# Optimization experiments

Measured on AMD Instinct MI355X. Metric: run time of the kernel, lower is better.

Reference implementation:

```python
import jax, jax.numpy as jnp
import numpy as np

# bitsandbytes NF4 codebook (16 quantile values in [-1, 1])
NF4 = jnp.array([
    -1.0, -0.6961928009986877, -0.5250730514526367, -0.39491748809814453,
    -0.28444138169288635, -0.18477343022823334, -0.09105003625154495, 0.0,
    0.07958029955625534, 0.16093020141124725, 0.24611230194568634,
    0.33791524171829224, 0.44070982933044434, 0.5626170039176941,
    0.7229568362236328, 1.0], dtype=jnp.float32)
BLOCK = 64  # bnb default quantization blocksize


def dequant_nf4(codes, absmax):
    """codes: int array of 4-bit indices, absmax: per-64-elem-block scale."""
    flat = NF4[codes.reshape(-1)]                      # codebook lookup
    flat = flat.reshape(-1, BLOCK) * absmax[:, None]   # per-block rescale
    return flat.reshape(codes.shape)


def setup_inputs() -> dict:
    key = jax.random.key(0)
    k1, k2, k3, k4, k5 = jax.random.split(key, 5)
    B, S, IN, OUT, R = 4, 2048, 4096, 4096, 8
    x = jax.random.normal(k1, (B, S, IN), dtype=jnp.float32)
    codes_A = jax.random.randint(k2, (R, IN), 0, 16, dtype=jnp.int32)
    absmax_A = jax.random.uniform(k3, (R * IN // BLOCK,), dtype=jnp.float32)
    codes_B = jax.random.randint(k4, (OUT, R), 0, 16, dtype=jnp.int32)
    absmax_B = jax.random.uniform(k5, (OUT * R // BLOCK,), dtype=jnp.float32)
    return {"x": x, "codes_A": codes_A, "absmax_A": absmax_A,
            "codes_B": codes_B, "absmax_B": absmax_B}


def reference(x, codes_A, absmax_A, codes_B, absmax_B):
    SCALING = 32.0 / 8.0  # alpha / rank
    W_A = dequant_nf4(codes_A, absmax_A)   # [rank, in]
    W_B = dequant_nf4(codes_B, absmax_B)   # [out, rank]
    interm = jnp.einsum('bsi,ri->bsr', x, W_A)          # lora_A: x @ W_A^T
    out = jnp.einsum('bsr,or->bso', interm, W_B)        # lora_B
    return out * SCALING
```

## Files before the change

kernel.cpp:

```cpp
#include <hip/hip_runtime.h>


static __device__ __constant__ float NF4_TBL[16] = {
    -1.0f, -0.6961928009986877f, -0.5250730514526367f, -0.39491748809814453f,
    -0.28444138169288635f, -0.18477343022823334f, -0.09105003625154495f, 0.0f,
    0.07958029955625534f, 0.16093020141124725f, 0.24611230194568634f,
    0.33791524171829224f, 0.44070982933044434f, 0.5626170039176941f,
    0.7229568362236328f, 1.0f};

__global__ void nf4_dequant_kernel(const int* __restrict__ codesA,
                                   const float* __restrict__ absA,
                                   const int* __restrict__ codesB,
                                   const float* __restrict__ absB,
                                   float* __restrict__ wA,
                                   float* __restrict__ wBt,
                                   int n) {
    int id = blockIdx.x * blockDim.x + threadIdx.x;
    if (id < n) {
        wA[id] = NF4_TBL[codesA[id] & 15] * absA[id >> 6];
        const int r = id >> 12;
        const int o = id & 4095;
        wBt[id] = NF4_TBL[codesB[o * 8 + r] & 15] * absB[o >> 3];
    }
}

__global__ __launch_bounds__(256) void lora_fused_kernel(
    const float* __restrict__ x,
    const float* __restrict__ wA,
    const float* __restrict__ wBt,
    float* __restrict__ out) {
    __shared__ float interm_s[8][8];

    const int t    = threadIdx.x;
    const int wave = t >> 6;
    const int lane = t & 63;
    const int row0 = blockIdx.x * 8;
    const int r0   = row0 + 2 * wave;

    const float4* __restrict__ x0  = (const float4*)(x + (size_t)r0 * 4096);
    const float4* __restrict__ x1  = x0 + 1024;
    const float4* __restrict__ wA4 = (const float4*)wA;

    float acc0[8], acc1[8];
    #pragma unroll
    for (int r = 0; r < 8; ++r) { acc0[r] = 0.f; acc1[r] = 0.f; }

    #pragma unroll 2
    for (int c = 0; c < 16; ++c) {
        const int idx = lane + 64 * c;
        const float4 xa = x0[idx];
        const float4 xb = x1[idx];
        #pragma unroll
        for (int r = 0; r < 8; ++r) {
            const float4 w = wA4[r * 1024 + idx];
            acc0[r] += xa.x * w.x + xa.y * w.y + xa.z * w.z + xa.w * w.w;
            acc1[r] += xb.x * w.x + xb.y * w.y + xb.z * w.z + xb.w * w.w;
        }
    }

    #pragma unroll
    for (int r = 0; r < 8; ++r) {
        float v0 = acc0[r], v1 = acc1[r];
        #pragma unroll
        for (int off = 32; off > 0; off >>= 1) {
            v0 += __shfl_down(v0, off, 64);
            v1 += __shfl_down(v1, off, 64);
        }
        if (lane == 0) {
            interm_s[2 * wave][r]     = v0;
            interm_s[2 * wave + 1][r] = v1;
        }
    }
    __syncthreads();

    float ims[8][8];
    #pragma unroll
    for (int m = 0; m < 8; ++m)
        #pragma unroll
        for (int r = 0; r < 8; ++r) {
            const float v = interm_s[m][r] * 4.0f;
            ims[m][r] = __int_as_float(
                __builtin_amdgcn_readfirstlane(__float_as_int(v)));
        }

    const float4* __restrict__ wt = (const float4*)wBt;

    #pragma unroll 1
    for (int k = 0; k < 4; ++k) {
        const int og = t + 256 * k;
        float4 w[8];
        #pragma unroll
        for (int r = 0; r < 8; ++r) w[r] = wt[r * 1024 + og];

        #pragma unroll
        for (int m = 0; m < 8; ++m) {
            float4 s;
            s.x = ims[m][0] * w[0].x + ims[m][1] * w[1].x + ims[m][2] * w[2].x
                + ims[m][3] * w[3].x + ims[m][4] * w[4].x + ims[m][5] * w[5].x
                + ims[m][6] * w[6].x + ims[m][7] * w[7].x;
            s.y = ims[m][0] * w[0].y + ims[m][1] * w[1].y + ims[m][2] * w[2].y
                + ims[m][3] * w[3].y + ims[m][4] * w[4].y + ims[m][5] * w[5].y
                + ims[m][6] * w[6].y + ims[m][7] * w[7].y;
            s.z = ims[m][0] * w[0].z + ims[m][1] * w[1].z + ims[m][2] * w[2].z
                + ims[m][3] * w[3].z + ims[m][4] * w[4].z + ims[m][5] * w[5].z
                + ims[m][6] * w[6].z + ims[m][7] * w[7].z;
            s.w = ims[m][0] * w[0].w + ims[m][1] * w[1].w + ims[m][2] * w[2].w
                + ims[m][3] * w[3].w + ims[m][4] * w[4].w + ims[m][5] * w[5].w
                + ims[m][6] * w[6].w + ims[m][7] * w[7].w;
            ((float4*)(out + (size_t)(row0 + m) * 4096))[og] = s;
        }
    }
}

extern "C" void kernel_launch(void* const* d_in, const int* in_sizes, int n_in,
                              void* d_out, int out_size, void* d_ws, size_t ws_size,
                              hipStream_t stream) {
    const float* x        = (const float*)d_in[0];
    const int*   codes_A  = (const int*)d_in[1];
    const float* absmax_A = (const float*)d_in[2];
    const int*   codes_B  = (const int*)d_in[3];
    const float* absmax_B = (const float*)d_in[4];
    float* out = (float*)d_out;

    constexpr int NW = 8 * 4096;
    float* wA  = (float*)d_ws;
    float* wBt = (float*)d_ws + NW;

    nf4_dequant_kernel<<<(NW + 255) / 256, 256, 0, stream>>>(
        codes_A, absmax_A, codes_B, absmax_B, wA, wBt, NW);

    lora_fused_kernel<<<8192 / 8, 256, 0, stream>>>(x, wA, wBt, out);
}
```

Baseline: 259.3 us.

## Split K dimension across waves with 16-lane row groups for lora_A stage

```diff
diff --git a/kernel.cpp b/kernel.cpp
--- a/kernel.cpp
+++ b/kernel.cpp
@@ -29,30 +29,33 @@
     const float* __restrict__ wA,
     const float* __restrict__ wBt,
     float* __restrict__ out) {
-    __shared__ float interm_s[8][8];
+    __shared__ float p_s[4][8][8];
+    __shared__ float im_s[8][8];
 
     const int t    = threadIdx.x;
     const int wave = t >> 6;
     const int lane = t & 63;
+    const int g    = lane >> 4;
+    const int l16  = lane & 15;
     const int row0 = blockIdx.x * 8;
-    const int r0   = row0 + 2 * wave;
 
-    const float4* __restrict__ x0  = (const float4*)(x + (size_t)r0 * 4096);
-    const float4* __restrict__ x1  = x0 + 1024;
-    const float4* __restrict__ wA4 = (const float4*)wA;
+    const float4* __restrict__ x0 =
+        (const float4*)(x + (size_t)(row0 + 2 * g) * 4096) + wave * 256;
+    const float4* __restrict__ x1 = x0 + 1024;
+    const float4* __restrict__ wq = (const float4*)wA + wave * 256;
 
     float acc0[8], acc1[8];
     #pragma unroll
     for (int r = 0; r < 8; ++r) { acc0[r] = 0.f; acc1[r] = 0.f; }
 
     #pragma unroll 2
-    for (int c = 0; c < 16; ++c) {
-        const int idx = lane + 64 * c;
+    for (int s = 0; s < 16; ++s) {
+        const int idx = s * 16 + l16;
         const float4 xa = x0[idx];
         const float4 xb = x1[idx];
         #pragma unroll
         for (int r = 0; r < 8; ++r) {
-            const float4 w = wA4[r * 1024 + idx];
+            const float4 w = wq[r * 1024 + idx];
             acc0[r] += xa.x * w.x + xa.y * w.y + xa.z * w.z + xa.w * w.w;
             acc1[r] += xb.x * w.x + xb.y * w.y + xb.z * w.z + xb.w * w.w;
         }
@@ -62,14 +65,21 @@
     for (int r = 0; r < 8; ++r) {
         float v0 = acc0[r], v1 = acc1[r];
         #pragma unroll
-        for (int off = 32; off > 0; off >>= 1) {
-            v0 += __shfl_down(v0, off, 64);
-            v1 += __shfl_down(v1, off, 64);
+        for (int off = 8; off > 0; off >>= 1) {
+            v0 += __shfl_down(v0, off, 16);
+            v1 += __shfl_down(v1, off, 16);
         }
-        if (lane == 0) {
-            interm_s[2 * wave][r]     = v0;
-            interm_s[2 * wave + 1][r] = v1;
+        if (l16 == 0) {
+            p_s[wave][2 * g][r]     = v0;
+            p_s[wave][2 * g + 1][r] = v1;
         }
+    }
+    __syncthreads();
+
+    if (t < 64) {
+        const int m = t >> 3, r = t & 7;
+        im_s[m][r] = (p_s[0][m][r] + p_s[1][m][r] +
+                      p_s[2][m][r] + p_s[3][m][r]) * 4.0f;
     }
     __syncthreads();
 
@@ -77,11 +87,9 @@
     #pragma unroll
     for (int m = 0; m < 8; ++m)
         #pragma unroll
-        for (int r = 0; r < 8; ++r) {
-            const float v = interm_s[m][r] * 4.0f;
+        for (int r = 0; r < 8; ++r)
             ims[m][r] = __int_as_float(
-                __builtin_amdgcn_readfirstlane(__float_as_int(v)));
-        }
+                __builtin_amdgcn_readfirstlane(__float_as_int(im_s[m][r])));
 
     const float4* __restrict__ wt = (const float4*)wBt;
 
```

Measured after the change: 257.1 us. No clear change (-0.9%).

## Split fused LoRA kernel into separate A-projection and B-projection kernels

Applied to the files above, without the earlier changes.

```diff
diff --git a/kernel.cpp b/kernel.cpp
--- a/kernel.cpp
+++ b/kernel.cpp
@@ -24,20 +24,15 @@
     }
 }
 
-__global__ __launch_bounds__(256) void lora_fused_kernel(
+__global__ __launch_bounds__(256) void lora_a_kernel(
     const float* __restrict__ x,
     const float* __restrict__ wA,
-    const float* __restrict__ wBt,
-    float* __restrict__ out) {
-    __shared__ float interm_s[8][8];
+    float* __restrict__ interm) {
+    const int lane = threadIdx.x & 63;
+    const int wid  = blockIdx.x * 4 + (threadIdx.x >> 6);
+    const size_t row0 = (size_t)wid * 2;
 
-    const int t    = threadIdx.x;
-    const int wave = t >> 6;
-    const int lane = t & 63;
-    const int row0 = blockIdx.x * 8;
-    const int r0   = row0 + 2 * wave;
-
-    const float4* __restrict__ x0  = (const float4*)(x + (size_t)r0 * 4096);
+    const float4* __restrict__ x0  = (const float4*)(x + row0 * 4096);
     const float4* __restrict__ x1  = x0 + 1024;
     const float4* __restrict__ wA4 = (const float4*)wA;
 
@@ -45,16 +40,16 @@
     #pragma unroll
     for (int r = 0; r < 8; ++r) { acc0[r] = 0.f; acc1[r] = 0.f; }
 
-    #pragma unroll 2
-    for (int c = 0; c < 16; ++c) {
-        const int idx = lane + 64 * c;
-        const float4 xa = x0[idx];
-        const float4 xb = x1[idx];
+    #pragma unroll 1
+    for (int q = 0; q < 16; ++q) {
+        const int idx = q * 64 + lane;
+        const float4 a0 = x0[idx];
+        const float4 a1 = x1[idx];
         #pragma unroll
         for (int r = 0; r < 8; ++r) {
             const float4 w = wA4[r * 1024 + idx];
-            acc0[r] += xa.x * w.x + xa.y * w.y + xa.z * w.z + xa.w * w.w;
-            acc1[r] += xb.x * w.x + xb.y * w.y + xb.z * w.z + xb.w * w.w;
+            acc0[r] += a0.x * w.x + a0.y * w.y + a0.z * w.z + a0.w * w.w;
+            acc1[r] += a1.x * w.x + a1.y * w.y + a1.z * w.z + a1.w * w.w;
         }
     }
 
@@ -67,23 +62,30 @@
             v1 += __shfl_down(v1, off, 64);
         }
         if (lane == 0) {
-            interm_s[2 * wave][r]     = v0;
-            interm_s[2 * wave + 1][r] = v1;
+            interm[row0 * 8 + r]       = v0 * 4.0f;
+            interm[(row0 + 1) * 8 + r] = v1 * 4.0f;
         }
     }
-    __syncthreads();
+}
 
-    float ims[8][8];
+__global__ __launch_bounds__(256) void lora_b_kernel(
+    const float* __restrict__ interm,
+    const float* __restrict__ wBt,
+    float* __restrict__ out) {
+    const int t    = threadIdx.x;
+    const size_t row0 = (size_t)blockIdx.x * 4;
+
+    const float* __restrict__ ip = interm + row0 * 8;
+    float ims[4][8];
     #pragma unroll
-    for (int m = 0; m < 8; ++m)
+    for (int m = 0; m < 4; ++m)
         #pragma unroll
-        for (int r = 0; r < 8; ++r) {
-            const float v = interm_s[m][r] * 4.0f;
+        for (int r = 0; r < 8; ++r)
             ims[m][r] = __int_as_float(
-                __builtin_amdgcn_readfirstlane(__float_as_int(v)));
-        }
+                __builtin_amdgcn_readfirstlane(__float_as_int(ip[m * 8 + r])));
 
     const float4* __restrict__ wt = (const float4*)wBt;
+    float4* __restrict__ o4 = (float4*)(out + row0 * 4096);
 
     #pragma unroll 1
     for (int k = 0; k < 4; ++k) {
@@ -93,7 +95,7 @@
         for (int r = 0; r < 8; ++r) w[r] = wt[r * 1024 + og];
 
         #pragma unroll
-        for (int m = 0; m < 8; ++m) {
+        for (int m = 0; m < 4; ++m) {
             float4 s;
             s.x = ims[m][0] * w[0].x + ims[m][1] * w[1].x + ims[m][2] * w[2].x
                 + ims[m][3] * w[3].x + ims[m][4] * w[4].x + ims[m][5] * w[5].x
@@ -107,7 +109,7 @@
             s.w = ims[m][0] * w[0].w + ims[m][1] * w[1].w + ims[m][2] * w[2].w
                 + ims[m][3] * w[3].w + ims[m][4] * w[4].w + ims[m][5] * w[5].w
                 + ims[m][6] * w[6].w + ims[m][7] * w[7].w;
-            ((float4*)(out + (size_t)(row0 + m) * 4096))[og] = s;
+            o4[m * 1024 + og] = s;
         }
     }
 }
@@ -123,11 +125,13 @@
     float* out = (float*)d_out;
 
     constexpr int NW = 8 * 4096;
-    float* wA  = (float*)d_ws;
-    float* wBt = (float*)d_ws + NW;
+    float* wA     = (float*)d_ws;
+    float* wBt    = (float*)d_ws + NW;
+    float* interm = (float*)d_ws + 2 * NW;
 
     nf4_dequant_kernel<<<(NW + 255) / 256, 256, 0, stream>>>(
         codes_A, absmax_A, codes_B, absmax_B, wA, wBt, NW);
 
-    lora_fused_kernel<<<8192 / 8, 256, 0, stream>>>(x, wA, wBt, out);
+    lora_a_kernel<<<1024, 256, 0, stream>>>(x, wA, interm);
+    lora_b_kernel<<<2048, 256, 0, stream>>>(interm, wBt, out);
 }
```

After: 254.5 us. Within noise of the previous version (-1.8%).
